# Kernel tuning notes

Measured on AMD Instinct MI355X. Metric: run time of the kernel, lower is better.

Reference implementation:

```python
import jax, jax.numpy as jnp
import numpy as np

D_MODEL = 2048
N_HEADS = 16
N_KV = 4
D_K = D_MODEL // N_HEADS  # 128
B, T = 2, 2048


def setup_inputs() -> dict:
    key = jax.random.key(0)
    ks = jax.random.split(key, 10)
    s = 1.0 / np.sqrt(D_MODEL)
    x = jax.random.normal(ks[0], (B, T, D_MODEL), dtype=jnp.float32)
    mask = jnp.ones((B, 1, T, T), dtype=bool)
    Wq = jax.random.uniform(ks[1], (D_MODEL, D_MODEL), minval=-s, maxval=s, dtype=jnp.float32)
    bq = jax.random.uniform(ks[2], (D_MODEL,), minval=-s, maxval=s, dtype=jnp.float32)
    Wk = jax.random.uniform(ks[3], (D_MODEL, N_KV * D_K), minval=-s, maxval=s, dtype=jnp.float32)
    bk = jax.random.uniform(ks[4], (N_KV * D_K,), minval=-s, maxval=s, dtype=jnp.float32)
    Wv = jax.random.uniform(ks[5], (D_MODEL, N_KV * D_K), minval=-s, maxval=s, dtype=jnp.float32)
    bv = jax.random.uniform(ks[6], (N_KV * D_K,), minval=-s, maxval=s, dtype=jnp.float32)
    Wo = jax.random.uniform(ks[7], (D_MODEL, D_MODEL), minval=-s, maxval=s, dtype=jnp.float32)
    bo = jax.random.uniform(ks[8], (D_MODEL,), minval=-s, maxval=s, dtype=jnp.float32)
    return {"x": x, "mask": mask, "Wq": Wq, "bq": bq, "Wk": Wk, "bk": bk,
            "Wv": Wv, "bv": bv, "Wo": Wo, "bo": bo}


def reference(x, mask, Wq, bq, Wk, bk, Wv, bv, Wo, bo):
    Bn, Tn, _ = x.shape
    g = N_HEADS // N_KV
    # projections
    q = (x @ Wq + bq).reshape(Bn, Tn, N_HEADS, D_K).transpose(0, 2, 1, 3)  # [B,H,T,d]
    k = (x @ Wk + bk).reshape(Bn, Tn, N_KV, D_K).transpose(0, 2, 1, 3)     # [B,Hk,T,d]
    v = (x @ Wv + bv).reshape(Bn, Tn, N_KV, D_K).transpose(0, 2, 1, 3)
    # GQA broadcast: group Q heads as [B,Hk,g,T,d]; no repeat_interleave copy
    qg = q.reshape(Bn, N_KV, g, Tn, D_K)
    scores = jnp.einsum('bkgqd,bkld->bkgql', qg, k) / jnp.sqrt(jnp.float32(D_K))
    scores = jnp.where(mask[:, :, None, :, :], scores, jnp.float32(-1e9))
    attn = jax.nn.softmax(scores, axis=-1)  # dropout=0 (eval)
    out = jnp.einsum('bkgql,bkld->bkgqd', attn, v)  # [B,Hk,g,T,d]
    out = out.reshape(Bn, N_HEADS, Tn, D_K).transpose(0, 2, 1, 3).reshape(Bn, Tn, D_MODEL)
    return out @ Wo + bo
```

## Files before the change

### kernel.cpp

```cpp
#include <hip/hip_runtime.h>
#include <hip/hip_bf16.h>

typedef __attribute__((ext_vector_type(8))) short short8;
typedef __attribute__((ext_vector_type(4))) short short4v;
typedef __attribute__((ext_vector_type(4))) float f32x4;
typedef __attribute__((ext_vector_type(16))) float f32x16;
typedef __attribute__((ext_vector_type(2))) unsigned uint2v;

__device__ __forceinline__ unsigned short f2bf(float f) {
  union { float f; unsigned u; } v; v.f = f;
  unsigned u = v.u;
  return (unsigned short)((u + 0x7fffu + ((u >> 16) & 1u)) >> 16);
}

__device__ __forceinline__ unsigned packbf2(float a, float b) {
  union { __hip_bfloat162 h; unsigned u; } c;
  c.h = __float22bfloat162_rn(float2{a, b});
  return c.u;
}

__device__ __forceinline__ void gload16(void* lds, const void* g) {
  __builtin_amdgcn_global_load_lds(
      (__attribute__((address_space(1))) unsigned int*)g,
      (__attribute__((address_space(3))) unsigned int*)lds, 16, 0, 0);
}

#define BAR() asm volatile("s_barrier" ::: "memory")
#define LGKM0() asm volatile("s_waitcnt lgkmcnt(0)" ::: "memory")

__global__ void cast_f32_bf16(const float* __restrict__ in,
                              unsigned short* __restrict__ out, int n8) {
  int i = blockIdx.x * 256 + threadIdx.x;
  if (i >= n8) return;
  const float4* p = (const float4*)in + (size_t)i * 2;
  float4 a = p[0], b = p[1];
  union { unsigned short u[8]; short8 v; } o;
  o.u[0] = f2bf(a.x); o.u[1] = f2bf(a.y); o.u[2] = f2bf(a.z); o.u[3] = f2bf(a.w);
  o.u[4] = f2bf(b.x); o.u[5] = f2bf(b.y); o.u[6] = f2bf(b.z); o.u[7] = f2bf(b.w);
  *(short8*)(out + (size_t)i * 8) = o.v;
}

__global__ void trans_cast(const float* __restrict__ src,
                           unsigned short* __restrict__ dst,
                           int N, int rowOff) {
  __shared__ float tile[32][33];
  int n0 = blockIdx.x * 32, k0 = blockIdx.y * 32;
  int c = threadIdx.x & 31, rr = threadIdx.x >> 5;
#pragma unroll
  for (int p = 0; p < 4; ++p) {
    int r = p * 8 + rr;
    tile[r][c] = src[(size_t)(k0 + r) * N + n0 + c];
  }
  __syncthreads();
#pragma unroll
  for (int p = 0; p < 4; ++p) {
    int r = p * 8 + rr;
    dst[(size_t)(rowOff + n0 + r) * 2048 + k0 + c] = f2bf(tile[c][r]);
  }
}

__global__ __launch_bounds__(512, 2) void gemm256(
    const unsigned short* __restrict__ A, const unsigned short* __restrict__ Bt,
    int K, int mode,
    const float* __restrict__ b0, const float* __restrict__ b1,
    const float* __restrict__ b2,
    unsigned short* __restrict__ oq, unsigned short* __restrict__ ok,
    unsigned short* __restrict__ ov, float* __restrict__ of) {
  __shared__ char L[131072];
  int tid = threadIdx.x, wid = tid >> 6, lane = tid & 63, lo = lane & 15, hi = lane >> 4;
  int wr = wid >> 2, wc = wid & 3;
  int m0 = blockIdx.x * 256, n0 = blockIdx.y * 256;
  const char* Ab = (const char*)A + (size_t)m0 * K * 2;
  const char* Bb = (const char*)Bt + (size_t)n0 * K * 2;
  f32x4 acc[8][4] = {};
  int NT = K >> 6;

  auto STAGE = [&](int p, int which, int kt) {
    const char* src = which ? Bb : Ab;
    char* dst = L + p * 65536 + which * 32768 + wid * 1024;
#pragma unroll
    for (int it = 0; it < 4; ++it) {
      int o = it * 8192 + wid * 1024 + lane * 16;
      int r = o >> 7;
      int cb = (o & 127) ^ ((r & 7) << 4);
      gload16(dst + it * 8192, src + (size_t)r * K * 2 + kt * 128 + cb);
    }
  };

  short8 af[2][4], bf0[2][2], bf1[2][2];

  STAGE(0, 0, 0); STAGE(0, 1, 0);
  STAGE(1, 0, 1); STAGE(1, 1, 1);
  asm volatile("s_waitcnt vmcnt(8)" ::: "memory");
  BAR();

  for (int t = 0; t < NT; ++t) {
    int p = t & 1;
    const char* AB = L + p * 65536;
    const char* BB = AB + 32768;

#pragma unroll
    for (int ks = 0; ks < 2; ++ks) {
#pragma unroll
      for (int i = 0; i < 4; ++i) {
        int row = wr * 128 + i * 16 + lo;
        af[ks][i] = *(const short8*)(AB + ((row * 128 + ks * 64 + hi * 16) ^ ((row & 7) << 4)));
      }
#pragma unroll
      for (int j = 0; j < 2; ++j) {
        int row = wc * 64 + j * 16 + lo;
        bf0[ks][j] = *(const short8*)(BB + ((row * 128 + ks * 64 + hi * 16) ^ ((row & 7) << 4)));
      }
    }
    BAR(); LGKM0();
    __builtin_amdgcn_s_setprio(1);
#pragma unroll
    for (int ks = 0; ks < 2; ++ks)
#pragma unroll
      for (int i = 0; i < 4; ++i)
#pragma unroll
        for (int j = 0; j < 2; ++j)
          acc[i][j] = __builtin_amdgcn_mfma_f32_16x16x32_bf16(af[ks][i], bf0[ks][j], acc[i][j], 0, 0, 0);
    __builtin_amdgcn_s_setprio(0);
    BAR();

#pragma unroll
    for (int ks = 0; ks < 2; ++ks)
#pragma unroll
      for (int j = 0; j < 2; ++j) {
        int row = wc * 64 + 32 + j * 16 + lo;
        bf1[ks][j] = *(const short8*)(BB + ((row * 128 + ks * 64 + hi * 16) ^ ((row & 7) << 4)));
      }
    BAR(); LGKM0();
    __builtin_amdgcn_s_setprio(1);
#pragma unroll
    for (int ks = 0; ks < 2; ++ks)
#pragma unroll
      for (int i = 0; i < 4; ++i)
#pragma unroll
        for (int j = 0; j < 2; ++j)
          acc[i][2 + j] = __builtin_amdgcn_mfma_f32_16x16x32_bf16(af[ks][i], bf1[ks][j], acc[i][2 + j], 0, 0, 0);
    __builtin_amdgcn_s_setprio(0);
    BAR();

#pragma unroll
    for (int ks = 0; ks < 2; ++ks)
#pragma unroll
      for (int i = 0; i < 4; ++i) {
        int row = wr * 128 + 64 + i * 16 + lo;
        af[ks][i] = *(const short8*)(AB + ((row * 128 + ks * 64 + hi * 16) ^ ((row & 7) << 4)));
      }
    if (t + 2 < NT) STAGE(p, 1, t + 2);
    BAR(); LGKM0();
    __builtin_amdgcn_s_setprio(1);
#pragma unroll
    for (int ks = 0; ks < 2; ++ks)
#pragma unroll
      for (int i = 0; i < 4; ++i)
#pragma unroll
        for (int j = 0; j < 2; ++j)
          acc[4 + i][2 + j] = __builtin_amdgcn_mfma_f32_16x16x32_bf16(af[ks][i], bf1[ks][j], acc[4 + i][2 + j], 0, 0, 0);
    __builtin_amdgcn_s_setprio(0);
    BAR();

    if (t + 2 < NT) STAGE(p, 0, t + 2);
    BAR();
    __builtin_amdgcn_s_setprio(1);
#pragma unroll
    for (int ks = 0; ks < 2; ++ks)
#pragma unroll
      for (int i = 0; i < 4; ++i)
#pragma unroll
        for (int j = 0; j < 2; ++j)
          acc[4 + i][j] = __builtin_amdgcn_mfma_f32_16x16x32_bf16(af[ks][i], bf0[ks][j], acc[4 + i][j], 0, 0, 0);
    __builtin_amdgcn_s_setprio(0);
    if (t == NT - 2) { asm volatile("s_waitcnt vmcnt(0)" ::: "memory"); }
    else            { asm volatile("s_waitcnt vmcnt(8)" ::: "memory"); }
    BAR();
  }

#pragma unroll
  for (int ii = 0; ii < 8; ++ii) {
    int mbase = m0 + wr * 128 + ii * 16 + hi * 4;
#pragma unroll
    for (int jj = 0; jj < 4; ++jj) {
      int n = n0 + wc * 64 + jj * 16 + lo;
      if (mode == 0) {
        float bias;
        if (n < 2048) bias = b0[n];
        else if (n < 2560) bias = b1[n - 2048];
        else bias = b2[n - 2560];
#pragma unroll
        for (int r = 0; r < 4; ++r) {
          int mm = mbase + r;
          int b = mm >> 11, t = mm & 2047;
          float val = acc[ii][jj][r] + bias;
          if (n < 2048) {
            int h = n >> 7, d = n & 127;
            oq[(((size_t)(b * 16 + h)) * 2048 + t) * 128 + d] =
                f2bf(val * (0.08838834764831845f * 1.4426950408889634f));
          } else if (n < 2560) {
            int kvh = (n - 2048) >> 7, d = (n - 2048) & 127;
            ok[(((size_t)(b * 4 + kvh)) * 2048 + t) * 128 + d] = f2bf(val);
          } else {
            int kvh = (n - 2560) >> 7, d = (n - 2560) & 127;
            ov[(((size_t)(b * 4 + kvh)) * 128 + d) * 2048 + t] = f2bf(val);
          }
        }
      } else {
        float bias = b0[n];
#pragma unroll
        for (int r = 0; r < 4; ++r)
          of[(size_t)(mbase + r) * 2048 + n] = acc[ii][jj][r] + bias;
      }
    }
  }
}

__device__ __forceinline__ void stageK(char* KLb, const char* kcb, int w, int lane, int t0) {
#pragma unroll
  for (int j = 0; j < 4; ++j) {
    int o = j * 4096 + w * 1024 + lane * 16;
    int row = o >> 8, col = o & 255;
    gload16(KLb + j * 4096 + w * 1024,
            kcb + (size_t)(t0 + row) * 256 + (col ^ ((row & 15) << 4)));
  }
}
__device__ __forceinline__ void stageV(char* VLb, const char* vcb, int w, int lane, int t0) {
#pragma unroll
  for (int j = 0; j < 4; ++j) {
    int o = j * 4096 + w * 1024 + lane * 16;
    int d = o >> 7, col = o & 127;
    gload16(VLb + j * 4096 + w * 1024,
            vcb + (size_t)d * 4096 + t0 * 2 + (col ^ ((d & 7) << 4)));
  }
}

__global__ __launch_bounds__(256, 2) void attn_fwd(
    const unsigned short* __restrict__ q, const unsigned short* __restrict__ kg,
    const unsigned short* __restrict__ vtg, unsigned short* __restrict__ attn) {
  __shared__ unsigned short kbuf[16384];
  __shared__ unsigned short vbuf[16384];
  int tid = threadIdx.x, w = tid >> 6, lane = tid & 63;
  int l31 = lane & 31, hi5 = lane >> 5;
  int tq0 = blockIdx.x * 128, h = blockIdx.y, b = blockIdx.z, kvh = h >> 2;
  int qrow = tq0 + w * 32;

  const unsigned short* qbase = q + ((size_t)(b * 16 + h)) * 2048 * 128;
  short8 qf[8];
#pragma unroll
  for (int ds_ = 0; ds_ < 8; ++ds_)
    qf[ds_] = *(const short8*)(qbase + (size_t)(qrow + l31) * 128 + ds_ * 16 + hi5 * 8);

  f32x16 oacc[4] = {};
  float mrow = -1e30f, lsum = 0.f;

  const char* kcb = (const char*)(kg + ((size_t)(b * 4 + kvh)) * 2048 * 128);
  const char* vcb = (const char*)(vtg + ((size_t)(b * 4 + kvh)) * 128 * 2048);
  char* KL = (char*)kbuf;
  char* VL = (char*)vbuf;

  stageK(KL, kcb, w, lane, 0);
  stageV(VL, vcb, w, lane, 0);
  __syncthreads();
  int buf = 0;

  for (int t0 = 0; t0 < 2048; t0 += 64) {
    if (t0 + 64 < 2048) {
      stageK(KL + (buf ^ 1) * 16384, kcb, w, lane, t0 + 64);
      stageV(VL + (buf ^ 1) * 16384, vcb, w, lane, t0 + 64);
    }
    const char* KB = KL + buf * 16384;
    const char* VB = VL + buf * 16384;

    f32x16 s[2] = {};
    __builtin_amdgcn_s_setprio(1);
#pragma unroll
    for (int ds_ = 0; ds_ < 8; ++ds_) {
#pragma unroll
      for (int f = 0; f < 2; ++f) {
        int row = f * 32 + l31;
        short8 kf = *(const short8*)(KB + ((row * 256 + ds_ * 32 + hi5 * 16) ^ ((row & 15) << 4)));
        s[f] = __builtin_amdgcn_mfma_f32_32x32x16_bf16(kf, qf[ds_], s[f], 0, 0, 0);
      }
    }
    __builtin_amdgcn_s_setprio(0);

    float am = fmaxf(s[0][0], s[0][1]);
#pragma unroll
    for (int r = 2; r < 16; ++r) am = fmaxf(am, s[0][r]);
#pragma unroll
    for (int r = 0; r < 16; ++r) am = fmaxf(am, s[1][r]);

    if (!__all(am <= mrow + 8.f)) {
      float ar = fmaxf(am, __shfl_xor(am, 32));
      float mnew = fmaxf(mrow, ar);
      float fsv = __builtin_amdgcn_exp2f(mrow - mnew);
      mrow = mnew;
      lsum *= fsv;
#pragma unroll
      for (int g = 0; g < 4; ++g)
#pragma unroll
        for (int r = 0; r < 4; ++r) {
          float fsr = __shfl(fsv, r + 8 * g + 4 * hi5);
#pragma unroll
          for (int db = 0; db < 4; ++db) oacc[db][4 * g + r] *= fsr;
        }
    }

    unsigned pk01[2][4], pk23[2][4];
    float accl = 0.f;
#pragma unroll
    for (int f = 0; f < 2; ++f)
#pragma unroll
      for (int g = 0; g < 4; ++g) {
        float p0 = __builtin_amdgcn_exp2f(s[f][4 * g + 0] - mrow);
        float p1 = __builtin_amdgcn_exp2f(s[f][4 * g + 1] - mrow);
        float p2 = __builtin_amdgcn_exp2f(s[f][4 * g + 2] - mrow);
        float p3 = __builtin_amdgcn_exp2f(s[f][4 * g + 3] - mrow);
        pk01[f][g] = packbf2(p0, p1);
        pk23[f][g] = packbf2(p2, p3);
        accl += (p0 + p1) + (p2 + p3);
      }
    lsum += accl;

    short8 pA[4];
#pragma unroll
    for (int f = 0; f < 2; ++f)
#pragma unroll
      for (int p = 0; p < 2; ++p) {
        uint2v a01 = __builtin_amdgcn_permlane32_swap(pk01[f][2 * p], pk01[f][2 * p + 1], false, false);
        uint2v a23 = __builtin_amdgcn_permlane32_swap(pk23[f][2 * p], pk23[f][2 * p + 1], false, false);
        union { unsigned u[4]; short8 v; } pa;
        pa.u[0] = a01.x; pa.u[1] = a23.x; pa.u[2] = a01.y; pa.u[3] = a23.y;
        pA[2 * f + p] = pa.v;
      }

    __builtin_amdgcn_s_setprio(1);
#pragma unroll
    for (int db = 0; db < 4; ++db) {
      int d = db * 32 + l31;
      int sw = (d & 7) << 4;
#pragma unroll
      for (int step = 0; step < 4; ++step) {
        short8 vf = *(const short8*)(VB + ((d * 128 + step * 32 + hi5 * 16) ^ sw));
        oacc[db] = __builtin_amdgcn_mfma_f32_32x32x16_bf16(pA[step], vf, oacc[db], 0, 0, 0);
      }
    }
    __builtin_amdgcn_s_setprio(0);
    __syncthreads();
    buf ^= 1;
  }

  unsigned short* ob = attn + ((size_t)b * 2048) * 2048 + h * 128;
  float ls = lsum + __shfl_xor(lsum, 32);
  float linv = 1.0f / ls;
#pragma unroll
  for (int g = 0; g < 4; ++g)
#pragma unroll
    for (int r = 0; r < 4; ++r) {
      float lr = __shfl(linv, r + 8 * g + 4 * hi5);
      int t = qrow + r + 8 * g + 4 * hi5;
#pragma unroll
      for (int db = 0; db < 4; ++db)
        ob[(size_t)t * 2048 + db * 32 + l31] = f2bf(oacc[db][4 * g + r] * lr);
    }
}

extern "C" void kernel_launch(void* const* d_in, const int* in_sizes, int n_in,
                              void* d_out, int out_size, void* d_ws, size_t ws_size,
                              hipStream_t stream) {
  const float* x  = (const float*)d_in[0];
  const float* Wq = (const float*)d_in[2];
  const float* bq = (const float*)d_in[3];
  const float* Wk = (const float*)d_in[4];
  const float* bk = (const float*)d_in[5];
  const float* Wv = (const float*)d_in[6];
  const float* bv = (const float*)d_in[7];
  const float* Wo = (const float*)d_in[8];
  const float* bo = (const float*)d_in[9];
  float* out = (float*)d_out;

  char* ws = (char*)d_ws;
  unsigned short* xb    = (unsigned short*)(ws);
  unsigned short* wqkvT = (unsigned short*)(ws + 16777216);
  unsigned short* woT   = (unsigned short*)(ws + 29360128);
  unsigned short* qb    = (unsigned short*)(ws + 37748736);
  unsigned short* kbw   = (unsigned short*)(ws + 54525952);
  unsigned short* vtw   = (unsigned short*)(ws + 58720256);
  unsigned short* attnb = (unsigned short*)(ws + 62914560);

  cast_f32_bf16<<<dim3(4096), dim3(256), 0, stream>>>(x, xb, 1048576);
  trans_cast<<<dim3(64, 64), dim3(256), 0, stream>>>(Wq, wqkvT, 2048, 0);
  trans_cast<<<dim3(16, 64), dim3(256), 0, stream>>>(Wk, wqkvT, 512, 2048);
  trans_cast<<<dim3(16, 64), dim3(256), 0, stream>>>(Wv, wqkvT, 512, 2560);
  trans_cast<<<dim3(64, 64), dim3(256), 0, stream>>>(Wo, woT, 2048, 0);

  gemm256<<<dim3(16, 12), dim3(512), 0, stream>>>(
      xb, wqkvT, 2048, 0, bq, bk, bv, qb, kbw, vtw, nullptr);

  attn_fwd<<<dim3(16, 16, 2), dim3(256), 0, stream>>>(qb, kbw, vtw, attnb);

  gemm256<<<dim3(16, 8), dim3(512), 0, stream>>>(
      attnb, woT, 2048, 1, bo, nullptr, nullptr, nullptr, nullptr, nullptr, out);
}
```

Measured before the change: 254.5 us.

## Fuse prep kernels, add 128x256 output GEMM, MFMA row-sums in attention

Merges the x cast and four weight transpose-casts into one launch to cut launch overhead. Adds a dedicated output-projection GEMM with 128-row tiles, giving 256 blocks instead of 128 for better CU fill on the 2048x2048 output. Re-splits the QKV GEMM's staging into finer chunks issued across more phases of the loop. In attention, the softmax row-sum is computed with an extra MFMA against a ones vector instead of scalar adds plus a shuffle, and the max reduction is restructured; this trades VALU work for extra matrix ops and bf16-rounded sums.

Measured after the change: 224.8 us. 11.7% less time.

```diff
diff --git a/kernel.cpp b/kernel.cpp
--- a/kernel.cpp
+++ b/kernel.cpp
@@ -2,7 +2,6 @@
 #include <hip/hip_bf16.h>
 
 typedef __attribute__((ext_vector_type(8))) short short8;
-typedef __attribute__((ext_vector_type(4))) short short4v;
 typedef __attribute__((ext_vector_type(4))) float f32x4;
 typedef __attribute__((ext_vector_type(16))) float f32x16;
 typedef __attribute__((ext_vector_type(2))) unsigned uint2v;
@@ -28,24 +27,31 @@
 #define BAR() asm volatile("s_barrier" ::: "memory")
 #define LGKM0() asm volatile("s_waitcnt lgkmcnt(0)" ::: "memory")
 
-__global__ void cast_f32_bf16(const float* __restrict__ in,
-                              unsigned short* __restrict__ out, int n8) {
-  int i = blockIdx.x * 256 + threadIdx.x;
-  if (i >= n8) return;
-  const float4* p = (const float4*)in + (size_t)i * 2;
-  float4 a = p[0], b = p[1];
-  union { unsigned short u[8]; short8 v; } o;
-  o.u[0] = f2bf(a.x); o.u[1] = f2bf(a.y); o.u[2] = f2bf(a.z); o.u[3] = f2bf(a.w);
-  o.u[4] = f2bf(b.x); o.u[5] = f2bf(b.y); o.u[6] = f2bf(b.z); o.u[7] = f2bf(b.w);
-  *(short8*)(out + (size_t)i * 8) = o.v;
-}
-
-__global__ void trans_cast(const float* __restrict__ src,
-                           unsigned short* __restrict__ dst,
-                           int N, int rowOff) {
+__global__ void prep(const float* __restrict__ x, const float* __restrict__ Wq,
+                     const float* __restrict__ Wk, const float* __restrict__ Wv,
+                     const float* __restrict__ Wo,
+                     unsigned short* __restrict__ xb,
+                     unsigned short* __restrict__ wqkvT,
+                     unsigned short* __restrict__ woT) {
+  int id = blockIdx.x, tid = threadIdx.x;
+  if (id < 4096) {
+    int i = id * 256 + tid;
+    const float4* p = (const float4*)x + (size_t)i * 2;
+    float4 a = p[0], b = p[1];
+    union { unsigned short u[8]; short8 v; } o;
+    o.u[0] = f2bf(a.x); o.u[1] = f2bf(a.y); o.u[2] = f2bf(a.z); o.u[3] = f2bf(a.w);
+    o.u[4] = f2bf(b.x); o.u[5] = f2bf(b.y); o.u[6] = f2bf(b.z); o.u[7] = f2bf(b.w);
+    *(short8*)(xb + (size_t)i * 8) = o.v;
+    return;
+  }
   __shared__ float tile[32][33];
-  int n0 = blockIdx.x * 32, k0 = blockIdx.y * 32;
-  int c = threadIdx.x & 31, rr = threadIdx.x >> 5;
+  const float* src; unsigned short* dst; int N, rowOff, tn, tk;
+  if (id < 8192)       { int t = id - 4096;  src = Wq; dst = wqkvT; N = 2048; rowOff = 0;    tn = t & 63; tk = t >> 6; }
+  else if (id < 9216)  { int t = id - 8192;  src = Wk; dst = wqkvT; N = 512;  rowOff = 2048; tn = t & 15; tk = t >> 4; }
+  else if (id < 10240) { int t = id - 9216;  src = Wv; dst = wqkvT; N = 512;  rowOff = 2560; tn = t & 15; tk = t >> 4; }
+  else                 { int t = id - 10240; src = Wo; dst = woT;   N = 2048; rowOff = 0;    tn = t & 63; tk = t >> 6; }
+  int n0 = tn * 32, k0 = tk * 32;
+  int c = tid & 31, rr = tid >> 5;
 #pragma unroll
   for (int p = 0; p < 4; ++p) {
     int r = p * 8 + rr;
@@ -61,11 +67,11 @@
 
 __global__ __launch_bounds__(512, 2) void gemm256(
     const unsigned short* __restrict__ A, const unsigned short* __restrict__ Bt,
-    int K, int mode,
+    int K,
     const float* __restrict__ b0, const float* __restrict__ b1,
     const float* __restrict__ b2,
     unsigned short* __restrict__ oq, unsigned short* __restrict__ ok,
-    unsigned short* __restrict__ ov, float* __restrict__ of) {
+    unsigned short* __restrict__ ov) {
   __shared__ char L[131072];
   int tid = threadIdx.x, wid = tid >> 6, lane = tid & 63, lo = lane & 15, hi = lane >> 4;
   int wr = wid >> 2, wc = wid & 3;
@@ -77,14 +83,22 @@
 
   auto STAGE = [&](int p, int which, int kt) {
     const char* src = which ? Bb : Ab;
-    char* dst = L + p * 65536 + which * 32768 + wid * 1024;
+    char* dstb = L + p * 65536 + which * 32768 + wid * 1024;
 #pragma unroll
     for (int it = 0; it < 4; ++it) {
       int o = it * 8192 + wid * 1024 + lane * 16;
       int r = o >> 7;
       int cb = (o & 127) ^ ((r & 7) << 4);
-      gload16(dst + it * 8192, src + (size_t)r * K * 2 + kt * 128 + cb);
-    }
+      gload16(dstb + it * 8192, src + (size_t)r * K * 2 + kt * 128 + cb);
+    }
+  };
+  auto STAGE1 = [&](int p, int which, int kt, int c) {
+    const char* src = which ? Bb : Ab;
+    int o = c * 1024 + lane * 16;
+    int r = o >> 7;
+    int cb = (o & 127) ^ ((r & 7) << 4);
+    gload16(L + p * 65536 + which * 32768 + c * 1024,
+            src + (size_t)r * K * 2 + kt * 128 + cb);
   };
 
   short8 af[2][4], bf0[2][2], bf1[2][2];
@@ -131,6 +145,7 @@
         int row = wc * 64 + 32 + j * 16 + lo;
         bf1[ks][j] = *(const short8*)(BB + ((row * 128 + ks * 64 + hi * 16) ^ ((row & 7) << 4)));
       }
+    if (t + 2 < NT) { STAGE1(p, 0, t + 2, wid); STAGE1(p, 0, t + 2, 16 + wid); }
     BAR(); LGKM0();
     __builtin_amdgcn_s_setprio(1);
 #pragma unroll
@@ -150,7 +165,7 @@
         int row = wr * 128 + 64 + i * 16 + lo;
         af[ks][i] = *(const short8*)(AB + ((row * 128 + ks * 64 + hi * 16) ^ ((row & 7) << 4)));
       }
-    if (t + 2 < NT) STAGE(p, 1, t + 2);
+    if (t + 2 < NT) { STAGE1(p, 1, t + 2, 2 * wid); STAGE1(p, 1, t + 2, 2 * wid + 1); }
     BAR(); LGKM0();
     __builtin_amdgcn_s_setprio(1);
 #pragma unroll
@@ -163,7 +178,10 @@
     __builtin_amdgcn_s_setprio(0);
     BAR();
 
-    if (t + 2 < NT) STAGE(p, 0, t + 2);
+    if (t + 2 < NT) {
+      STAGE1(p, 0, t + 2, 8 + wid);  STAGE1(p, 0, t + 2, 24 + wid);
+      STAGE1(p, 1, t + 2, 16 + 2 * wid); STAGE1(p, 1, t + 2, 17 + 2 * wid);
+    }
     BAR();
     __builtin_amdgcn_s_setprio(1);
 #pragma unroll
@@ -175,7 +193,7 @@
           acc[4 + i][j] = __builtin_amdgcn_mfma_f32_16x16x32_bf16(af[ks][i], bf0[ks][j], acc[4 + i][j], 0, 0, 0);
     __builtin_amdgcn_s_setprio(0);
     if (t == NT - 2) { asm volatile("s_waitcnt vmcnt(0)" ::: "memory"); }
-    else            { asm volatile("s_waitcnt vmcnt(8)" ::: "memory"); }
+    else             { asm volatile("s_waitcnt vmcnt(8)" ::: "memory"); }
     BAR();
   }
 
@@ -185,34 +203,134 @@
 #pragma unroll
     for (int jj = 0; jj < 4; ++jj) {
       int n = n0 + wc * 64 + jj * 16 + lo;
-      if (mode == 0) {
-        float bias;
-        if (n < 2048) bias = b0[n];
-        else if (n < 2560) bias = b1[n - 2048];
-        else bias = b2[n - 2560];
-#pragma unroll
-        for (int r = 0; r < 4; ++r) {
-          int mm = mbase + r;
-          int b = mm >> 11, t = mm & 2047;
-          float val = acc[ii][jj][r] + bias;
-          if (n < 2048) {
-            int h = n >> 7, d = n & 127;
-            oq[(((size_t)(b * 16 + h)) * 2048 + t) * 128 + d] =
-                f2bf(val * (0.08838834764831845f * 1.4426950408889634f));
-          } else if (n < 2560) {
-            int kvh = (n - 2048) >> 7, d = (n - 2048) & 127;
-            ok[(((size_t)(b * 4 + kvh)) * 2048 + t) * 128 + d] = f2bf(val);
-          } else {
-            int kvh = (n - 2560) >> 7, d = (n - 2560) & 127;
-            ov[(((size_t)(b * 4 + kvh)) * 128 + d) * 2048 + t] = f2bf(val);
-          }
+      float bias;
+      if (n < 2048) bias = b0[n];
+      else if (n < 2560) bias = b1[n - 2048];
+      else bias = b2[n - 2560];
+#pragma unroll
+      for (int r = 0; r < 4; ++r) {
+        int mm = mbase + r;
+        int b = mm >> 11, t = mm & 2047;
+        float val = acc[ii][jj][r] + bias;
+        if (n < 2048) {
+          int h = n >> 7, d = n & 127;
+          oq[(((size_t)(b * 16 + h)) * 2048 + t) * 128 + d] =
+              f2bf(val * (0.08838834764831845f * 1.4426950408889634f));
+        } else if (n < 2560) {
+          int kvh = (n - 2048) >> 7, d = (n - 2048) & 127;
+          ok[(((size_t)(b * 4 + kvh)) * 2048 + t) * 128 + d] = f2bf(val);
+        } else {
+          int kvh = (n - 2560) >> 7, d = (n - 2560) & 127;
+          ov[(((size_t)(b * 4 + kvh)) * 128 + d) * 2048 + t] = f2bf(val);
         }
-      } else {
-        float bias = b0[n];
-#pragma unroll
-        for (int r = 0; r < 4; ++r)
-          of[(size_t)(mbase + r) * 2048 + n] = acc[ii][jj][r] + bias;
-      }
+      }
+    }
+  }
+}
+
+__global__ __launch_bounds__(512, 2) void gemmO(
+    const unsigned short* __restrict__ A, const unsigned short* __restrict__ Bt,
+    int K, const float* __restrict__ bias, float* __restrict__ of) {
+  __shared__ char L[98304];
+  int tid = threadIdx.x, wid = tid >> 6, lane = tid & 63, lo = lane & 15, hi = lane >> 4;
+  int wr = wid >> 2, wc = wid & 3;
+  int m0 = blockIdx.x * 128, n0 = blockIdx.y * 256;
+  const char* Ab = (const char*)A + (size_t)m0 * K * 2;
+  const char* Bb = (const char*)Bt + (size_t)n0 * K * 2;
+  f32x4 acc[4][4] = {};
+  int NT = K >> 6;
+
+  auto SA = [&](int p, int kt, int c) {
+    int o = c * 1024 + lane * 16;
+    int r = o >> 7;
+    int cb = (o & 127) ^ ((r & 7) << 4);
+    gload16(L + p * 49152 + c * 1024, Ab + (size_t)r * K * 2 + kt * 128 + cb);
+  };
+  auto SB = [&](int p, int kt, int c) {
+    int o = c * 1024 + lane * 16;
+    int r = o >> 7;
+    int cb = (o & 127) ^ ((r & 7) << 4);
+    gload16(L + p * 49152 + 16384 + c * 1024, Bb + (size_t)r * K * 2 + kt * 128 + cb);
+  };
+  int ev0 = (wid & 3) + (wid >> 2) * 8, ev1 = 16 + ev0;
+  int od0 = 4 + (wid & 3) + (wid >> 2) * 8, od1 = 16 + od0;
+
+  SA(0, 0, 2 * wid); SA(0, 0, 2 * wid + 1);
+  SB(0, 0, ev0); SB(0, 0, ev1); SB(0, 0, od0); SB(0, 0, od1);
+  SA(1, 1, 2 * wid); SA(1, 1, 2 * wid + 1); SB(1, 1, ev0); SB(1, 1, ev1);
+  asm volatile("s_waitcnt vmcnt(4)" ::: "memory");
+  BAR();
+
+  for (int t = 0; t < NT; ++t) {
+    int p = t & 1;
+    const char* AB = L + p * 49152;
+    const char* BB = AB + 16384;
+    short8 af[2][4], bf0[2][2], bf1[2][2];
+
+#pragma unroll
+    for (int ks = 0; ks < 2; ++ks) {
+#pragma unroll
+      for (int i = 0; i < 4; ++i) {
+        int row = wr * 64 + i * 16 + lo;
+        af[ks][i] = *(const short8*)(AB + ((row * 128 + ks * 64 + hi * 16) ^ ((row & 7) << 4)));
+      }
+#pragma unroll
+      for (int j = 0; j < 2; ++j) {
+        int row = wc * 64 + j * 16 + lo;
+        bf0[ks][j] = *(const short8*)(BB + ((row * 128 + ks * 64 + hi * 16) ^ ((row & 7) << 4)));
+      }
+    }
+    if (t + 1 < NT) { SB(p ^ 1, t + 1, od0); SB(p ^ 1, t + 1, od1); }
+    BAR(); LGKM0();
+    __builtin_amdgcn_s_setprio(1);
+#pragma unroll
+    for (int ks = 0; ks < 2; ++ks)
+#pragma unroll
+      for (int i = 0; i < 4; ++i)
+#pragma unroll
+        for (int j = 0; j < 2; ++j)
+          acc[i][j] = __builtin_amdgcn_mfma_f32_16x16x32_bf16(af[ks][i], bf0[ks][j], acc[i][j], 0, 0, 0);
+    __builtin_amdgcn_s_setprio(0);
+    if (t >= NT - 3) { asm volatile("s_waitcnt vmcnt(0)" ::: "memory"); }
+    else             { asm volatile("s_waitcnt vmcnt(6)" ::: "memory"); }
+    BAR();
+
+#pragma unroll
+    for (int ks = 0; ks < 2; ++ks)
+#pragma unroll
+      for (int j = 0; j < 2; ++j) {
+        int row = wc * 64 + 32 + j * 16 + lo;
+        bf1[ks][j] = *(const short8*)(BB + ((row * 128 + ks * 64 + hi * 16) ^ ((row & 7) << 4)));
+      }
+    if (t + 2 < NT) {
+      SA(p, t + 2, 2 * wid); SA(p, t + 2, 2 * wid + 1);
+      SB(p, t + 2, ev0); SB(p, t + 2, ev1);
+    }
+    BAR(); LGKM0();
+    __builtin_amdgcn_s_setprio(1);
+#pragma unroll
+    for (int ks = 0; ks < 2; ++ks)
+#pragma unroll
+      for (int i = 0; i < 4; ++i)
+#pragma unroll
+        for (int j = 0; j < 2; ++j)
+          acc[i][2 + j] = __builtin_amdgcn_mfma_f32_16x16x32_bf16(af[ks][i], bf1[ks][j], acc[i][2 + j], 0, 0, 0);
+    __builtin_amdgcn_s_setprio(0);
+    if (t >= NT - 3) { asm volatile("s_waitcnt vmcnt(0)" ::: "memory"); }
+    else             { asm volatile("s_waitcnt vmcnt(6)" ::: "memory"); }
+    BAR();
+  }
+
+#pragma unroll
+  for (int ii = 0; ii < 4; ++ii) {
+    int mbase = m0 + wr * 64 + ii * 16 + hi * 4;
+#pragma unroll
+    for (int jj = 0; jj < 4; ++jj) {
+      int n = n0 + wc * 64 + jj * 16 + lo;
+      float bv = bias[n];
+#pragma unroll
+      for (int r = 0; r < 4; ++r)
+        of[(size_t)(mbase + r) * 2048 + n] = acc[ii][jj][r] + bv;
     }
   }
 }
@@ -253,7 +371,9 @@
     qf[ds_] = *(const short8*)(qbase + (size_t)(qrow + l31) * 128 + ds_ * 16 + hi5 * 8);
 
   f32x16 oacc[4] = {};
-  float mrow = -1e30f, lsum = 0.f;
+  f32x16 lacc = {};
+  float mrow = -1e30f;
+  const short8 onesv = {16256, 16256, 16256, 16256, 16256, 16256, 16256, 16256};
 
   const char* kcb = (const char*)(kg + ((size_t)(b * 4 + kvh)) * 2048 * 128);
   const char* vcb = (const char*)(vtg + ((size_t)(b * 4 + kvh)) * 128 * 2048);
@@ -288,28 +408,28 @@
 
     float am = fmaxf(s[0][0], s[0][1]);
 #pragma unroll
-    for (int r = 2; r < 16; ++r) am = fmaxf(am, s[0][r]);
-#pragma unroll
-    for (int r = 0; r < 16; ++r) am = fmaxf(am, s[1][r]);
+    for (int r = 2; r < 14; r += 2) am = fmaxf(fmaxf(am, s[0][r]), s[0][r + 1]);
+    am = fmaxf(fmaxf(am, s[0][14]), s[0][15]);
+#pragma unroll
+    for (int r = 0; r < 16; r += 2) am = fmaxf(fmaxf(am, s[1][r]), s[1][r + 1]);
 
     if (!__all(am <= mrow + 8.f)) {
       float ar = fmaxf(am, __shfl_xor(am, 32));
       float mnew = fmaxf(mrow, ar);
       float fsv = __builtin_amdgcn_exp2f(mrow - mnew);
       mrow = mnew;
-      lsum *= fsv;
 #pragma unroll
       for (int g = 0; g < 4; ++g)
 #pragma unroll
         for (int r = 0; r < 4; ++r) {
           float fsr = __shfl(fsv, r + 8 * g + 4 * hi5);
+          lacc[4 * g + r] *= fsr;
 #pragma unroll
           for (int db = 0; db < 4; ++db) oacc[db][4 * g + r] *= fsr;
         }
     }
 
     unsigned pk01[2][4], pk23[2][4];
-    float accl = 0.f;
 #pragma unroll
     for (int f = 0; f < 2; ++f)
 #pragma unroll
@@ -320,9 +440,7 @@
         float p3 = __builtin_amdgcn_exp2f(s[f][4 * g + 3] - mrow);
         pk01[f][g] = packbf2(p0, p1);
         pk23[f][g] = packbf2(p2, p3);
-        accl += (p0 + p1) + (p2 + p3);
-      }
-    lsum += accl;
+      }
 
     short8 pA[4];
 #pragma unroll
@@ -347,19 +465,20 @@
         oacc[db] = __builtin_amdgcn_mfma_f32_32x32x16_bf16(pA[step], vf, oacc[db], 0, 0, 0);
       }
     }
+#pragma unroll
+    for (int step = 0; step < 4; ++step)
+      lacc = __builtin_amdgcn_mfma_f32_32x32x16_bf16(pA[step], onesv, lacc, 0, 0, 0);
     __builtin_amdgcn_s_setprio(0);
     __syncthreads();
     buf ^= 1;
   }
 
   unsigned short* ob = attn + ((size_t)b * 2048) * 2048 + h * 128;
-  float ls = lsum + __shfl_xor(lsum, 32);
-  float linv = 1.0f / ls;
 #pragma unroll
   for (int g = 0; g < 4; ++g)
 #pragma unroll
     for (int r = 0; r < 4; ++r) {
-      float lr = __shfl(linv, r + 8 * g + 4 * hi5);
+      float lr = 1.0f / lacc[4 * g + r];
       int t = qrow + r + 8 * g + 4 * hi5;
 #pragma unroll
       for (int db = 0; db < 4; ++db)
@@ -390,17 +509,12 @@
   unsigned short* vtw   = (unsigned short*)(ws + 58720256);
   unsigned short* attnb = (unsigned short*)(ws + 62914560);
 
-  cast_f32_bf16<<<dim3(4096), dim3(256), 0, stream>>>(x, xb, 1048576);
-  trans_cast<<<dim3(64, 64), dim3(256), 0, stream>>>(Wq, wqkvT, 2048, 0);
-  trans_cast<<<dim3(16, 64), dim3(256), 0, stream>>>(Wk, wqkvT, 512, 2048);
-  trans_cast<<<dim3(16, 64), dim3(256), 0, stream>>>(Wv, wqkvT, 512, 2560);
-  trans_cast<<<dim3(64, 64), dim3(256), 0, stream>>>(Wo, woT, 2048, 0);
+  prep<<<dim3(14336), dim3(256), 0, stream>>>(x, Wq, Wk, Wv, Wo, xb, wqkvT, woT);
 
   gemm256<<<dim3(16, 12), dim3(512), 0, stream>>>(
-      xb, wqkvT, 2048, 0, bq, bk, bv, qb, kbw, vtw, nullptr);
+      xb, wqkvT, 2048, bq, bk, bv, qb, kbw, vtw);
 
   attn_fwd<<<dim3(16, 16, 2), dim3(256), 0, stream>>>(qb, kbw, vtw, attnb);
 
-  gemm256<<<dim3(16, 8), dim3(512), 0, stream>>>(
-      attnb, woT, 2048, 1, bo, nullptr, nullptr, nullptr, nullptr, nullptr, out);
-}
+  gemmO<<<dim3(32, 8), dim3(512), 0, stream>>>(attnb, woT, 2048, bo, out);
+}
```
